# Performance work log

Hardware: AMD Instinct MI355X
Metric: run time of the kernel (lower is better)

Reference implementation:

```python
import jax, jax.numpy as jnp
import numpy as np

EMBED = 1024
HEADS = 16
HEAD_DIM = EMBED // HEADS


def _rope(t):
    # t: (B, S, H, D) -> rotary embedding applied over last dim (GPT-NeoX rotate-half)
    B, S, H, D = t.shape
    half = D // 2
    inv_freq = 1.0 / (10000.0 ** (jnp.arange(0, half, dtype=jnp.float32) / half))
    freqs = jnp.arange(S, dtype=jnp.float32)[:, None] * inv_freq[None, :]  # (S, half)
    cos = jnp.cos(freqs)[None, :, None, :]
    sin = jnp.sin(freqs)[None, :, None, :]
    t1, t2 = t[..., :half], t[..., half:]
    return jnp.concatenate([t1 * cos - t2 * sin, t2 * cos + t1 * sin], axis=-1)


def setup_inputs() -> dict:
    key = jax.random.key(0)
    k1, k2, k3 = jax.random.split(key, 3)
    B, S = 2, 2048
    x = jax.random.normal(k1, (B, S, EMBED), dtype=jnp.float32)
    attn_mask = jnp.ones((B, S), dtype=bool)
    w_qkv = jax.random.normal(k2, (EMBED, 3 * EMBED), dtype=jnp.float32) * (1.0 / np.sqrt(EMBED))
    w_out = jax.random.normal(k3, (EMBED, EMBED), dtype=jnp.float32) * (1.0 / np.sqrt(EMBED))
    return {"x": x, "attn_mask": attn_mask, "w_qkv": w_qkv, "w_out": w_out, "is_causal": 1}


def reference(x, attn_mask, w_qkv, w_out, is_causal):
    B, S, E = x.shape
    qkv = x @ w_qkv                                   # (B, S, 3E)
    q, k, v = jnp.split(qkv, 3, axis=-1)
    q = q.reshape(B, S, HEADS, HEAD_DIM)
    k = k.reshape(B, S, HEADS, HEAD_DIM)
    v = v.reshape(B, S, HEADS, HEAD_DIM)
    q = _rope(q)
    k = _rope(k)
    scale = 1.0 / np.sqrt(HEAD_DIM)
    scores = jnp.einsum('bqhd,bkhd->bhqk', q, k) * scale  # (B, H, S, S)
    neg = jnp.asarray(-1e30, dtype=scores.dtype)
    if is_causal:
        causal = jnp.tril(jnp.ones((S, S), dtype=bool))
        scores = jnp.where(causal[None, None], scores, neg)
    else:
        scores = jnp.where(attn_mask[:, None, None, :], scores, neg)
    attn = jax.nn.softmax(scores, axis=-1)
    y = jnp.einsum('bhqk,bkhd->bqhd', attn, v).reshape(B, S, E)
    return y @ w_out
```

## Files before the change

### kernel.cpp

```cpp
#include <hip/hip_runtime.h>
#include <hip/hip_bf16.h>
#include <stdint.h>

typedef float v4f __attribute__((ext_vector_type(4)));
typedef short v8s __attribute__((ext_vector_type(8)));

#define LOG2E 1.44269504088896f
#define QSCALE (0.125f * LOG2E)
#define SOFTMAX_OFF 16.0f

__device__ __forceinline__ unsigned short f2bf(float f) {
    unsigned int u = __float_as_uint(f);
    u += 0x7fffu + ((u >> 16) & 1u);
    return (unsigned short)(u >> 16);
}

#define LDS_FENCE() __builtin_amdgcn_fence(__ATOMIC_ACQ_REL, "workgroup")

__device__ __forceinline__ void gload_lds16(const unsigned short* g, unsigned short* s) {
    __builtin_amdgcn_global_load_lds(
        (const __attribute__((address_space(1))) unsigned int*)g,
        (__attribute__((address_space(3))) unsigned int*)s, 16, 0, 0);
}

#define BAR()      asm volatile("s_barrier" ::: "memory")
#define VMWAIT(N)  asm volatile("s_waitcnt vmcnt(" #N ")" ::: "memory")
#define LGKM0()    do { asm volatile("s_waitcnt lgkmcnt(0)" ::: "memory"); \
                        __builtin_amdgcn_sched_barrier(0); } while (0)

#define PIPE_BARRIER_KEEP4()                                   \
    do {                                                       \
        asm volatile("s_waitcnt vmcnt(4)" ::: "memory");       \
        __builtin_amdgcn_s_barrier();                          \
        asm volatile("" ::: "memory");                         \
    } while (0)
#define PIPE_BARRIER_DRAIN()                                   \
    do {                                                       \
        asm volatile("s_waitcnt vmcnt(0)" ::: "memory");       \
        __builtin_amdgcn_s_barrier();                          \
        asm volatile("" ::: "memory");                         \
    } while (0)

__global__ void k_prep(const float* __restrict__ x,
                       const float* __restrict__ w_qkv,
                       const float* __restrict__ w_out,
                       unsigned short* __restrict__ xb,
                       unsigned short* __restrict__ wqkvT,
                       unsigned short* __restrict__ woutT,
                       float2* __restrict__ rope) {
    __shared__ unsigned short tile[64][65];
    int id = blockIdx.x, t = threadIdx.x;
    if (id < 1024) {
        int base = id * 256 + t;
#pragma unroll
        for (int k = 0; k < 4; ++k) {
            int i = base + k * 262144;
            float4 v = ((const float4*)x)[i];
            ushort4 o;
            o.x = f2bf(v.x); o.y = f2bf(v.y); o.z = f2bf(v.z); o.w = f2bf(v.w);
            ((ushort4*)xb)[i] = o;
        }
        return;
    }
    id -= 1024;
    if (id < 256) {
        int idx = id * 256 + t;
        int s = idx >> 5, d = idx & 31;
        float inv = __expf(-(float)d * 0.28782313662425572f);
        float sn, cs;
        sincosf((float)s * inv, &sn, &cs);
        rope[idx] = make_float2(cs, sn);
        return;
    }
    id -= 256;
    const float* src; unsigned short* dst; int N, kb, nb;
    if (id < 768) { src = w_qkv; dst = wqkvT; N = 3072; nb = (id % 48) * 64; kb = (id / 48) * 64; }
    else { id -= 768; src = w_out; dst = woutT; N = 1024; nb = (id % 16) * 64; kb = (id / 16) * 64; }
    const int K = 1024;
    for (int i = 0; i < 16; ++i) {
        int e = t + i * 256;
        int n_l = e & 63, k_l = e >> 6;
        tile[n_l][k_l] = f2bf(src[(size_t)(kb + k_l) * N + nb + n_l]);
    }
    __syncthreads();
    for (int i = 0; i < 16; ++i) {
        int e = t + i * 256;
        int k_l = e & 63, n_l = e >> 6;
        dst[(size_t)(nb + n_l) * K + kb + k_l] = tile[n_l][k_l];
    }
}

__global__ __launch_bounds__(512, 2) void k_gemm_qkv(
    const unsigned short* __restrict__ A,
    const unsigned short* __restrict__ Bt,
    const float2* __restrict__ rope,
    unsigned short* __restrict__ Qg,
    unsigned short* __restrict__ Kg,
    unsigned short* __restrict__ Vt) {
    const int K = 1024;
    __shared__ __align__(16) union {
        struct { unsigned short Ab[2][256 * 64], Bb[2][256 * 64]; } g;
        unsigned short vt[4][64][264];
        unsigned short qk[8][128][66];
    } sm;
    const int t = threadIdx.x;
    const int w = t >> 6, l = t & 63, quad = l >> 4, ln = l & 15;
    const int wr = w >> 2, wc = w & 3;
    const int mb = blockIdx.y * 256, nb = blockIdx.x * 256;
    const int lxr = l >> 3;
    const int swz = ((l & 7) ^ lxr) * 8;

    v4f acc[8][4];
#pragma unroll
    for (int i = 0; i < 8; ++i)
#pragma unroll
        for (int j = 0; j < 4; ++j) acc[i][j] = (v4f){0.f, 0.f, 0.f, 0.f};

    auto stageHT = [&](const unsigned short* src, int grow, int k0, unsigned short* lds) {
#pragma unroll
        for (int c = 0; c < 2; ++c) {
            int r0 = w * 16 + c * 8;
            gload_lds16(src + (size_t)(grow + r0 + lxr) * K + k0 + swz, lds + r0 * 64);
        }
    };
    auto frag = [&](const unsigned short* base, int row, int g16) -> v8s {
        return *(const v8s*)&base[row * 64 + ((g16 ^ (row & 7)) << 3)];
    };

    v8s aF[4][2], bF0[2][2], bF1[2][2];
    auto readA = [&](const unsigned short* Ap, int ih) {
#pragma unroll
        for (int ii = 0; ii < 4; ++ii) {
            int row = wr * 128 + (ih * 4 + ii) * 16 + ln;
#pragma unroll
            for (int kh = 0; kh < 2; ++kh) aF[ii][kh] = frag(Ap, row, kh * 4 + quad);
        }
    };
    auto readB = [&](const unsigned short* Bp, int jh, v8s (&bF)[2][2]) {
#pragma unroll
        for (int jj = 0; jj < 2; ++jj) {
            int row = wc * 64 + (jh * 2 + jj) * 16 + ln;
#pragma unroll
            for (int kh = 0; kh < 2; ++kh) bF[jj][kh] = frag(Bp, row, kh * 4 + quad);
        }
    };
    auto mfma16 = [&](v8s (&bF)[2][2], int ih, int jh) {
        __builtin_amdgcn_s_setprio(1);
#pragma unroll
        for (int ii = 0; ii < 4; ++ii)
#pragma unroll
            for (int jj = 0; jj < 2; ++jj) {
                v4f* ac = &acc[ih * 4 + ii][jh * 2 + jj];
                *ac = __builtin_amdgcn_mfma_f32_16x16x32_bf16(aF[ii][0], bF[jj][0], *ac, 0, 0, 0);
                *ac = __builtin_amdgcn_mfma_f32_16x16x32_bf16(aF[ii][1], bF[jj][1], *ac, 0, 0, 0);
            }
        __builtin_amdgcn_s_setprio(0);
        __builtin_amdgcn_sched_barrier(0);
    };

    const unsigned short* Ap0 = &sm.g.Ab[0][0];
    const unsigned short* Ap1 = &sm.g.Ab[1][0];
    const unsigned short* Bp0 = &sm.g.Bb[0][0];
    const unsigned short* Bp1 = &sm.g.Bb[1][0];

    stageHT(A,  mb,       0,  &sm.g.Ab[0][0]);
    stageHT(A,  mb + 128, 0,  &sm.g.Ab[0][128 * 64]);
    stageHT(Bt, nb,       0,  &sm.g.Bb[0][0]);
    stageHT(Bt, nb + 128, 0,  &sm.g.Bb[0][128 * 64]);
    stageHT(Bt, nb,       64, &sm.g.Bb[1][0]);
    stageHT(Bt, nb + 128, 64, &sm.g.Bb[1][128 * 64]);
    VMWAIT(4);
    BAR();

    for (int it = 0; it < 8; ++it) {
        const int c1k = (2 * it + 1) * 64, n0k = (2 * it + 2) * 64, n1k = (2 * it + 3) * 64;
        const bool pre = it < 7;
        readA(Ap0, 0); readB(Bp0, 0, bF0);
        stageHT(A, mb, c1k, &sm.g.Ab[1][0]);
        BAR(); LGKM0();
        mfma16(bF0, 0, 0);
        BAR();
        readB(Bp0, 1, bF1);
        stageHT(A, mb + 128, c1k, &sm.g.Ab[1][128 * 64]);
        BAR(); LGKM0();
        mfma16(bF1, 0, 1);
        BAR();
        readA(Ap0, 1);
        if (pre) stageHT(Bt, nb, n0k, &sm.g.Bb[0][0]);
        BAR(); LGKM0();
        mfma16(bF0, 1, 0);
        BAR();
        if (pre) stageHT(Bt, nb + 128, n0k, &sm.g.Bb[0][128 * 64]);
        BAR();
        mfma16(bF1, 1, 1);
        if (pre) VMWAIT(4); else VMWAIT(0);
        BAR();
        readA(Ap1, 0); readB(Bp1, 0, bF0);
        if (pre) stageHT(A, mb, n0k, &sm.g.Ab[0][0]);
        BAR(); LGKM0();
        mfma16(bF0, 0, 0);
        BAR();
        readB(Bp1, 1, bF1);
        if (pre) stageHT(A, mb + 128, n0k, &sm.g.Ab[0][128 * 64]);
        BAR(); LGKM0();
        mfma16(bF1, 0, 1);
        BAR();
        readA(Ap1, 1);
        if (pre) stageHT(Bt, nb, n1k, &sm.g.Bb[1][0]);
        BAR(); LGKM0();
        mfma16(bF0, 1, 0);
        BAR();
        if (pre) stageHT(Bt, nb + 128, n1k, &sm.g.Bb[1][128 * 64]);
        BAR();
        mfma16(bF1, 1, 1);
        if (pre) VMWAIT(4);
        BAR();
    }

    if (nb >= 2048) {
        __syncthreads();
#pragma unroll
        for (int i = 0; i < 8; ++i)
#pragma unroll
            for (int j = 0; j < 4; ++j) {
                int d = j * 16 + ln;
                int s0 = wr * 128 + i * 16 + quad * 4;
                ushort4 pk;
                pk.x = f2bf(acc[i][j][0]); pk.y = f2bf(acc[i][j][1]);
                pk.z = f2bf(acc[i][j][2]); pk.w = f2bf(acc[i][j][3]);
                *(ushort4*)&sm.vt[wc][d][s0] = pk;
            }
        __syncthreads();
        const int hbase = (nb & 1023) >> 6;
        const int b = mb >> 11, sbase = mb & 2047;
#pragma unroll
        for (int i = 0; i < 16; ++i) {
            int c = t + i * 512;
            int h2 = c >> 11, dd = (c >> 5) & 63, off = (c & 31) * 8;
            v8s val = *(const v8s*)&sm.vt[h2][dd][off];
            *(v8s*)(Vt + ((size_t)((b * 16 + hbase + h2) * 64 + dd) * 2048 + sbase + off)) = val;
        }
        return;
    }

    const int nbw = nb + wc * 64;
    const int region = nbw >> 10;
    const int h = (nbw & 1023) >> 6;
    unsigned short* dst = region == 0 ? Qg : Kg;
    const float scale = region == 0 ? QSCALE : 1.0f;
    unsigned short* qkw = &sm.qk[w][0][0];
#pragma unroll
    for (int jj = 0; jj < 2; ++jj) {
        const float2* rp = rope + jj * 16 + ln;
#pragma unroll
        for (int i = 0; i < 8; ++i)
#pragma unroll
            for (int r = 0; r < 4; ++r) {
                int lr = i * 16 + quad * 4 + r;
                int s = (mb + wr * 128 + lr) & 2047;
                float2 cs = rp[s * 32];
                float t1 = acc[i][jj][r], t2 = acc[i][jj + 2][r];
                qkw[lr * 66 + jj * 16 + ln]      = f2bf((t1 * cs.x - t2 * cs.y) * scale);
                qkw[lr * 66 + jj * 16 + ln + 32] = f2bf((t2 * cs.x + t1 * cs.y) * scale);
            }
    }
    LDS_FENCE();
    const int row0 = mb + wr * 128;
    const int bb = row0 >> 11, s0 = row0 & 2047;
    unsigned short* gbase = dst + ((size_t)(bb * 16 + h) * 2048 + s0) * 64;
#pragma unroll
    for (int itn = 0; itn < 16; ++itn) {
        int c = itn * 64 + l;
        int lr = c >> 3, off = (c & 7) * 8;
        v8s val = *(const v8s*)&qkw[lr * 66 + off];
        *(v8s*)(gbase + (size_t)lr * 64 + off) = val;
    }
}

__global__ __launch_bounds__(256) void k_gemm_out(
    const unsigned short* __restrict__ A,
    const unsigned short* __restrict__ Bt,
    float* __restrict__ C) {
    const int K = 1024, N = 1024;
    __shared__ __align__(16) unsigned short Ab[3][4096];
    __shared__ __align__(16) unsigned short Bb[3][4096];
    const int t = threadIdx.x;
    const int w = t >> 6, l = t & 63, quad = l >> 4, ln = l & 15;
    const int wm = (w >> 1) * 64, wn = (w & 1) * 64;
    const int mb = blockIdx.y * 128, nb = blockIdx.x * 128;

    v4f acc[4][4];
#pragma unroll
    for (int i = 0; i < 4; ++i)
#pragma unroll
        for (int j = 0; j < 4; ++j) acc[i][j] = (v4f){0.f, 0.f, 0.f, 0.f};

    auto stage = [&](int buf, int k0) {
#pragma unroll
        for (int u = 0; u < 2; ++u) {
            int e = t + u * 256;
            gload_lds16(A + (size_t)(mb + (e >> 2)) * K + k0 + (e & 3) * 8,
                        &Ab[buf][(w * 64 + u * 256) * 8]);
            gload_lds16(Bt + (size_t)(nb + (e >> 2)) * K + k0 + (e & 3) * 8,
                        &Bb[buf][(w * 64 + u * 256) * 8]);
        }
    };

    stage(0, 0);
    stage(1, 32);
    int cur = 0, nxt = 2;
    for (int itk = 0; itk < 32; ++itk) {
        if (itk < 31) PIPE_BARRIER_KEEP4();
        else          PIPE_BARRIER_DRAIN();
        if (itk + 2 < 32) {
            stage(nxt, (itk + 2) * 32);
            nxt = nxt == 2 ? 0 : nxt + 1;
        }
        v8s af[4], bfr[4];
#pragma unroll
        for (int i = 0; i < 4; ++i)
            af[i] = *(const v8s*)&Ab[cur][(wm + i * 16 + ln) * 32 + quad * 8];
#pragma unroll
        for (int j = 0; j < 4; ++j)
            bfr[j] = *(const v8s*)&Bb[cur][(wn + j * 16 + ln) * 32 + quad * 8];
#pragma unroll
        for (int i = 0; i < 4; ++i)
#pragma unroll
            for (int j = 0; j < 4; ++j)
                acc[i][j] = __builtin_amdgcn_mfma_f32_16x16x32_bf16(
                    af[i], bfr[j], acc[i][j], 0, 0, 0);
        cur = cur == 2 ? 0 : cur + 1;
    }

#pragma unroll
    for (int i = 0; i < 4; ++i) {
        int r0 = mb + wm + i * 16 + quad * 4;
#pragma unroll
        for (int j = 0; j < 4; ++j) {
            int c0 = nb + wn + j * 16 + ln;
#pragma unroll
            for (int r = 0; r < 4; ++r)
                C[(size_t)(r0 + r) * N + c0] = acc[i][j][r];
        }
    }
}

__global__ __launch_bounds__(256, 4) void k_flash(
    const unsigned short* __restrict__ Qg,
    const unsigned short* __restrict__ Kg,
    const unsigned short* __restrict__ Vt,
    unsigned short* __restrict__ Og) {
    __shared__ __align__(16) unsigned short Kb[2][64 * 64];
    __shared__ __align__(16) unsigned short Vb[2][64 * 64];

    const int id = blockIdx.x;
    const int xcd = id & 7, slot = id >> 3;
    const int bh = xcd * 4 + (slot & 3);
    const int qt = 31 - (slot >> 2);
    const int qbase = qt * 64;
    const int nit = qt + 1;

    const int t = threadIdx.x, w = t >> 6, l = t & 63, quad = l >> 4, ln = l & 15;
    const int b = bh >> 4, h = bh & 15;

    const unsigned short* Qp = Qg + (size_t)bh * 2048 * 64;
    const unsigned short* Kp = Kg + (size_t)bh * 2048 * 64;
    const unsigned short* Vp = Vt + (size_t)bh * 64 * 2048;

    unsigned kst[2], vst[2];
    int cchunk = l & 7, rloc = l >> 3;
#pragma unroll
    for (int j = 0; j < 2; ++j) {
        int c = w + j * 4;
        int rr = c * 8 + rloc;
        int g = (cchunk + rr) & 7;
        kst[j] = (unsigned)(rr * 64 + g * 8);
        vst[j] = (unsigned)(rr * 2048 + g * 8);
    }
    const int c0 = ((quad - ln) & 7) * 8;
    const int c1 = ((quad + 4 - ln) & 7) * 8;
    const v8s ones = {0x3F80, 0x3F80, 0x3F80, 0x3F80, 0x3F80, 0x3F80, 0x3F80, 0x3F80};

    const int qrow = qbase + w * 16 + ln;
    v8s qf0 = *(const v8s*)(Qp + (size_t)qrow * 64 + quad * 8);
    v8s qf1 = *(const v8s*)(Qp + (size_t)qrow * 64 + quad * 8 + 32);

    v4f oacc[5];
#pragma unroll
    for (int dt = 0; dt < 5; ++dt) oacc[dt] = (v4f){0.f, 0.f, 0.f, 0.f};

    auto stage = [&](int buf, int kvb) {
        const unsigned short* kg = Kp + (size_t)kvb * 64;
        const unsigned short* vg = Vp + kvb;
#pragma unroll
        for (int j = 0; j < 2; ++j) {
            int c = w + j * 4;
            gload_lds16(kg + kst[j], &Kb[buf][c * 512]);
            gload_lds16(vg + vst[j], &Vb[buf][c * 512]);
        }
    };

    auto compute = [&](int buf, int it) {
        v4f sc[4];
#pragma unroll
        for (int kt = 0; kt < 4; ++kt) {
            int row = kt * 16 + ln;
            v8s k0 = *(const v8s*)&Kb[buf][row * 64 + c0];
            v8s k1 = *(const v8s*)&Kb[buf][row * 64 + c1];
            sc[kt] = (v4f){0.f, 0.f, 0.f, 0.f};
            sc[kt] = __builtin_amdgcn_mfma_f32_16x16x32_bf16(qf0, k0, sc[kt], 0, 0, 0);
            sc[kt] = __builtin_amdgcn_mfma_f32_16x16x32_bf16(qf1, k1, sc[kt], 0, 0, 0);
        }
        if (it == qt) {
            int q0 = qbase + w * 16 + quad * 4;
#pragma unroll
            for (int kt = 0; kt < 4; ++kt) {
                int kv = qbase + kt * 16 + ln;
#pragma unroll
                for (int r = 0; r < 4; ++r)
                    if (kv > q0 + r) sc[kt][r] = -1e30f;
            }
        }
#pragma unroll
        for (int kt = 0; kt < 4; ++kt)
#pragma unroll
            for (int r = 0; r < 4; ++r)
                sc[kt][r] = exp2f(sc[kt][r] - SOFTMAX_OFF);

        BAR();
        unsigned short* Pw = &Kb[buf][w * 1024];
        const int gcol = ln & 7;
#pragma unroll
        for (int kt = 0; kt < 4; ++kt) {
            union { __hip_bfloat162 hh; unsigned int u; } p01, p23;
            p01.hh = __float22bfloat162_rn(make_float2(sc[kt][0], sc[kt][1]));
            p23.hh = __float22bfloat162_rn(make_float2(sc[kt][2], sc[kt][3]));
            int gq = kt * 2 + (ln >> 3);
            int r0w = quad * 4;
            Pw[(r0w + 0) * 64 + ((gq ^ ((r0w + 0) & 7)) << 3) + gcol] = (unsigned short)p01.u;
            Pw[(r0w + 1) * 64 + ((gq ^ ((r0w + 1) & 7)) << 3) + gcol] = (unsigned short)(p01.u >> 16);
            Pw[(r0w + 2) * 64 + ((gq ^ ((r0w + 2) & 7)) << 3) + gcol] = (unsigned short)p23.u;
            Pw[(r0w + 3) * 64 + ((gq ^ ((r0w + 3) & 7)) << 3) + gcol] = (unsigned short)(p23.u >> 16);
        }
        LDS_FENCE();
        v8s pf0 = *(const v8s*)&Pw[ln * 64 + ((quad ^ (ln & 7)) << 3)];
        v8s pf1 = *(const v8s*)&Pw[ln * 64 + (((quad + 4) ^ (ln & 7)) << 3)];
        LDS_FENCE();
        __builtin_amdgcn_s_setprio(1);
#pragma unroll
        for (int dt = 0; dt < 4; ++dt) {
            int row = dt * 16 + ln;
            v8s v0 = *(const v8s*)&Vb[buf][row * 64 + c0];
            v8s v1 = *(const v8s*)&Vb[buf][row * 64 + c1];
            oacc[dt] = __builtin_amdgcn_mfma_f32_16x16x32_bf16(pf0, v0, oacc[dt], 0, 0, 0);
            oacc[dt] = __builtin_amdgcn_mfma_f32_16x16x32_bf16(pf1, v1, oacc[dt], 0, 0, 0);
        }
        oacc[4] = __builtin_amdgcn_mfma_f32_16x16x32_bf16(pf0, ones, oacc[4], 0, 0, 0);
        oacc[4] = __builtin_amdgcn_mfma_f32_16x16x32_bf16(pf1, ones, oacc[4], 0, 0, 0);
        __builtin_amdgcn_s_setprio(0);
    };

    stage(0, 0);
    for (int it = 0;;) {
        const int buf = it & 1;
        stage(buf ^ 1, (it + 1) * 64);
        VMWAIT(4);
        BAR();
        compute(buf, it);
        if (++it >= nit) break;
        BAR();
    }

    float rden[4];
#pragma unroll
    for (int r = 0; r < 4; ++r) rden[r] = 1.f / oacc[4][r];
#pragma unroll
    for (int dt = 0; dt < 4; ++dt)
#pragma unroll
        for (int r = 0; r < 4; ++r) {
            int s = qbase + w * 16 + quad * 4 + r;
            Og[(size_t)(b * 2048 + s) * 1024 + h * 64 + dt * 16 + ln] =
                f2bf(oacc[dt][r] * rden[r]);
        }
}

extern "C" void kernel_launch(void* const* d_in, const int* in_sizes, int n_in,
                              void* d_out, int out_size, void* d_ws, size_t ws_size,
                              hipStream_t stream) {
    const float* x     = (const float*)d_in[0];
    const float* w_qkv = (const float*)d_in[2];
    const float* w_out = (const float*)d_in[3];
    char* ws = (char*)d_ws;

    unsigned short* xb    = (unsigned short*)(ws);
    unsigned short* wqkvT = (unsigned short*)(ws + (size_t)(8 << 20));
    unsigned short* woutT = (unsigned short*)(ws + (size_t)(14 << 20));
    unsigned short* Qg    = (unsigned short*)(ws + (size_t)(16 << 20));
    unsigned short* Kg    = (unsigned short*)(ws + (size_t)(24 << 20));
    unsigned short* Vt    = (unsigned short*)(ws + (size_t)(32 << 20));
    unsigned short* Og    = (unsigned short*)(ws + (size_t)(40 << 20));
    float2*         rope  = (float2*)(ws + (size_t)(48 << 20));

    k_prep<<<2304, 256, 0, stream>>>(x, w_qkv, w_out, xb, wqkvT, woutT, rope);
    k_gemm_qkv<<<dim3(12, 16), 512, 0, stream>>>(xb, wqkvT, rope, Qg, Kg, Vt);
    k_flash<<<1024, 256, 0, stream>>>(Qg, Kg, Vt, Og);
    k_gemm_out<<<dim3(8, 32), 256, 0, stream>>>(Og, woutT, (float*)d_out);
}
```

Measured before the change: 190.3 us.

## Keep attention probabilities in registers via transposed QK MFMA and swizzle GEMM block order

```diff
diff --git a/kernel.cpp b/kernel.cpp
--- a/kernel.cpp
+++ b/kernel.cpp
@@ -4,6 +4,7 @@
 
 typedef float v4f __attribute__((ext_vector_type(4)));
 typedef short v8s __attribute__((ext_vector_type(8)));
+typedef short v4s __attribute__((ext_vector_type(4)));
 
 #define LOG2E 1.44269504088896f
 #define QSCALE (0.125f * LOG2E)
@@ -106,7 +107,9 @@
     const int t = threadIdx.x;
     const int w = t >> 6, l = t & 63, quad = l >> 4, ln = l & 15;
     const int wr = w >> 2, wc = w & 3;
-    const int mb = blockIdx.y * 256, nb = blockIdx.x * 256;
+    const int lid = blockIdx.y * 12 + blockIdx.x;
+    const int swzb = (lid & 7) * 24 + (lid >> 3);
+    const int mb = (swzb / 12) * 256, nb = (swzb % 12) * 256;
     const int lxr = l >> 3;
     const int swz = ((l & 7) ^ lxr) * 8;
 
@@ -379,7 +382,11 @@
     }
     const int c0 = ((quad - ln) & 7) * 8;
     const int c1 = ((quad + 4 - ln) & 7) * 8;
-    const v8s ones = {0x3F80, 0x3F80, 0x3F80, 0x3F80, 0x3F80, 0x3F80, 0x3F80, 0x3F80};
+    int vcol[4];
+#pragma unroll
+    for (int kt = 0; kt < 4; ++kt)
+        vcol[kt] = (((kt * 2 + (quad >> 1) - ln) & 7) << 3) + (quad & 1) * 4;
+    const v4s ones4 = {0x3F80, 0x3F80, 0x3F80, 0x3F80};
 
     const int qrow = qbase + w * 16 + ln;
     v8s qf0 = *(const v8s*)(Qp + (size_t)qrow * 64 + quad * 8);
@@ -408,17 +415,17 @@
             v8s k0 = *(const v8s*)&Kb[buf][row * 64 + c0];
             v8s k1 = *(const v8s*)&Kb[buf][row * 64 + c1];
             sc[kt] = (v4f){0.f, 0.f, 0.f, 0.f};
-            sc[kt] = __builtin_amdgcn_mfma_f32_16x16x32_bf16(qf0, k0, sc[kt], 0, 0, 0);
-            sc[kt] = __builtin_amdgcn_mfma_f32_16x16x32_bf16(qf1, k1, sc[kt], 0, 0, 0);
+            sc[kt] = __builtin_amdgcn_mfma_f32_16x16x32_bf16(k0, qf0, sc[kt], 0, 0, 0);
+            sc[kt] = __builtin_amdgcn_mfma_f32_16x16x32_bf16(k1, qf1, sc[kt], 0, 0, 0);
         }
         if (it == qt) {
-            int q0 = qbase + w * 16 + quad * 4;
+            int qg = w * 16 + ln;
 #pragma unroll
             for (int kt = 0; kt < 4; ++kt) {
-                int kv = qbase + kt * 16 + ln;
+                int kv = kt * 16 + quad * 4;
 #pragma unroll
                 for (int r = 0; r < 4; ++r)
-                    if (kv > q0 + r) sc[kt][r] = -1e30f;
+                    if (kv + r > qg) sc[kt][r] = -1e30f;
             }
         }
 #pragma unroll
@@ -427,36 +434,29 @@
             for (int r = 0; r < 4; ++r)
                 sc[kt][r] = exp2f(sc[kt][r] - SOFTMAX_OFF);
 
-        BAR();
-        unsigned short* Pw = &Kb[buf][w * 1024];
-        const int gcol = ln & 7;
+        v4s pa[4];
 #pragma unroll
         for (int kt = 0; kt < 4; ++kt) {
             union { __hip_bfloat162 hh; unsigned int u; } p01, p23;
             p01.hh = __float22bfloat162_rn(make_float2(sc[kt][0], sc[kt][1]));
             p23.hh = __float22bfloat162_rn(make_float2(sc[kt][2], sc[kt][3]));
-            int gq = kt * 2 + (ln >> 3);
-            int r0w = quad * 4;
-            Pw[(r0w + 0) * 64 + ((gq ^ ((r0w + 0) & 7)) << 3) + gcol] = (unsigned short)p01.u;
-            Pw[(r0w + 1) * 64 + ((gq ^ ((r0w + 1) & 7)) << 3) + gcol] = (unsigned short)(p01.u >> 16);
-            Pw[(r0w + 2) * 64 + ((gq ^ ((r0w + 2) & 7)) << 3) + gcol] = (unsigned short)p23.u;
-            Pw[(r0w + 3) * 64 + ((gq ^ ((r0w + 3) & 7)) << 3) + gcol] = (unsigned short)(p23.u >> 16);
-        }
-        LDS_FENCE();
-        v8s pf0 = *(const v8s*)&Pw[ln * 64 + ((quad ^ (ln & 7)) << 3)];
-        v8s pf1 = *(const v8s*)&Pw[ln * 64 + (((quad + 4) ^ (ln & 7)) << 3)];
-        LDS_FENCE();
+            union { v4s v; unsigned int u[2]; } pk;
+            pk.u[0] = p01.u; pk.u[1] = p23.u;
+            pa[kt] = pk.v;
+        }
         __builtin_amdgcn_s_setprio(1);
 #pragma unroll
         for (int dt = 0; dt < 4; ++dt) {
-            int row = dt * 16 + ln;
-            v8s v0 = *(const v8s*)&Vb[buf][row * 64 + c0];
-            v8s v1 = *(const v8s*)&Vb[buf][row * 64 + c1];
-            oacc[dt] = __builtin_amdgcn_mfma_f32_16x16x32_bf16(pf0, v0, oacc[dt], 0, 0, 0);
-            oacc[dt] = __builtin_amdgcn_mfma_f32_16x16x32_bf16(pf1, v1, oacc[dt], 0, 0, 0);
-        }
-        oacc[4] = __builtin_amdgcn_mfma_f32_16x16x32_bf16(pf0, ones, oacc[4], 0, 0, 0);
-        oacc[4] = __builtin_amdgcn_mfma_f32_16x16x32_bf16(pf1, ones, oacc[4], 0, 0, 0);
+            int rowb = (dt * 16 + ln) * 64;
+#pragma unroll
+            for (int kt = 0; kt < 4; ++kt) {
+                v4s vf = *(const v4s*)&Vb[buf][rowb + vcol[kt]];
+                oacc[dt] = __builtin_amdgcn_mfma_f32_16x16x16bf16_1k(pa[kt], vf, oacc[dt], 0, 0, 0);
+            }
+        }
+#pragma unroll
+        for (int kt = 0; kt < 4; ++kt)
+            oacc[4] = __builtin_amdgcn_mfma_f32_16x16x16bf16_1k(pa[kt], ones4, oacc[4], 0, 0, 0);
         __builtin_amdgcn_s_setprio(0);
     };
 
```

Measured after the change: 186.7 us. About the same (-1.9%).
